# Optimization experiments

Hardware: AMD Instinct MI355X
Metric: run time of the kernel (lower is better)

Reference implementation:

```python
import jax, jax.numpy as jnp
import numpy as np

N_IN, N_LAT, LEN_T, N_SHIFT = 128, 21, 51, 50
N_HID, BATCH = 4, 2048


def identity_init(n_rows, n_cols):
    A = np.zeros((n_rows, n_cols), np.float32)
    if n_rows >= n_cols:
        k = n_rows - n_cols + 1
        for c in range(n_cols):
            A[c:c + k, c] = 1.0 / k
    else:
        k = n_cols - n_rows + 1
        for r in range(n_rows):
            A[r, r:r + k] = 1.0 / k
    return jnp.asarray(A)


def setup_inputs() -> dict:
    key = jax.random.key(0)
    ks = jax.random.split(key, 8)
    s = 0.05
    return {
        'inputs': jax.random.normal(ks[0], (BATCH, LEN_T, N_IN), dtype=jnp.float32),
        'enc_W': jax.random.normal(ks[1], (N_HID, N_IN, N_IN), dtype=jnp.float32) * s,
        'enc_b': jnp.zeros((N_HID, N_IN), jnp.float32),
        'enc_Wout': jax.random.normal(ks[2], (N_IN, N_IN), dtype=jnp.float32) * s,
        'enc_bout': jnp.zeros((N_IN,), jnp.float32),
        'dec_W': jax.random.normal(ks[3], (N_HID, N_IN, N_IN), dtype=jnp.float32) * s,
        'dec_b': jnp.zeros((N_HID, N_IN), jnp.float32),
        'dec_Wout': jax.random.normal(ks[4], (N_IN, N_IN), dtype=jnp.float32) * s,
        'dec_bout': jnp.zeros((N_IN,), jnp.float32),
        'W_enc_inner': identity_init(N_IN, N_LAT),
        'L': jnp.eye(N_LAT, dtype=jnp.float32),
        'W_dec_inner': identity_init(N_LAT, N_IN),
    }


def res_block(x, Ws, bs, Wout, bout):
    # DenseResBlock: ReLU hidden dense stack + linear output + identity skip
    h = x
    for i in range(Ws.shape[0]):
        h = jax.nn.relu(h @ Ws[i] + bs[i])
    return h @ Wout + bout + x


def reference(inputs, enc_W, enc_b, enc_Wout, enc_bout,
              dec_W, dec_b, dec_Wout, dec_bout,
              W_enc_inner, L, W_dec_inner):
    B = inputs.shape[0]
    len_pred = LEN_T - N_SHIFT  # = 1

    # ---- autoencoder branch (all timesteps flattened into rows) ----
    auto_in = inputs.reshape(-1, N_IN)                       # [B*T, n_in]
    part_enc = res_block(auto_in, enc_W, enc_b, enc_Wout, enc_bout)
    full_enc = part_enc @ W_enc_inner                        # [B*T, n_lat]
    part_dec = full_enc @ W_dec_inner                        # [B*T, n_in]
    autoencoder_output = res_block(part_dec, dec_W, dec_b, dec_Wout, dec_bout)
    autoencoder_output = autoencoder_output.reshape(B, LEN_T, N_IN)
    outer_auto_output = res_block(part_enc, dec_W, dec_b, dec_Wout, dec_bout)
    outer_auto_output = outer_auto_output.reshape(B, LEN_T, N_IN)

    # ---- prediction branch: recurrent application of Koopman operator L ----
    pred_in = inputs[:, :len_pred, :].reshape(-1, N_IN)      # [B*len_pred, n_in]
    cur = res_block(pred_in, enc_W, enc_b, enc_Wout, enc_bout) @ W_enc_inner

    def step(cur_enc, _):
        adv = cur_enc @ L                                    # [B*len_pred, n_lat]
        dec = res_block(adv @ W_dec_inner, dec_W, dec_b, dec_Wout, dec_bout)
        return adv, dec

    _, preds = jax.lax.scan(step, cur, None, length=N_SHIFT)  # [S, B*lp, n_in]
    preds = preds.reshape(N_SHIFT, B, len_pred, N_IN)
    predictions = preds.transpose(1, 0, 2, 3).reshape(B, N_SHIFT * len_pred, N_IN)

    return autoencoder_output, outer_auto_output, predictions
```

## Files before the change

kernel.cpp:

```cpp
#include <hip/hip_runtime.h>
#include <stdint.h>


typedef _Float16 h8 __attribute__((ext_vector_type(8)));
typedef _Float16 h4 __attribute__((ext_vector_type(4)));
typedef float    f4 __attribute__((ext_vector_type(4)));

#define ROWS_AUTO 104448
#define NT64      1632
#define NUNITS    1952

#define WT_ENCW      0
#define WT_ENCWOUT   (4*16384)
#define WT_DECW      (5*16384)
#define WT_DECWOUT   (9*16384)
#define WT_COMB      (10*16384)

#define MFULL_OFF_B 0x60000
#define ACH_OFF_B   0x200000
#define PE_OFF_B    0x220000
#define PET0_OFF_B  0x1C00000

#define H0 0
#define H1 16384
#define H2 32768
#define H3 49152
#define LDSE 51712
#define LDSD 68096

#define hsw(rl, c) ((rl)*256 + ((((c)) ^ ((rl) & 7)) << 4))

#define PIN(B) asm volatile("" : "+v"(B[0]), "+v"(B[1]), "+v"(B[2]), "+v"(B[3]), \
                                 "+v"(B[4]), "+v"(B[5]), "+v"(B[6]), "+v"(B[7]))

__device__ __forceinline__ f4 mfma16(h8 a, h8 b, f4 c) {
  return __builtin_amdgcn_mfma_f32_16x16x32_f16(a, b, c, 0, 0, 0);
}
__device__ __forceinline__ h8 cvt8(f4 a, f4 b) {
  h8 r;
  r[0]=(_Float16)a[0]; r[1]=(_Float16)a[1]; r[2]=(_Float16)a[2]; r[3]=(_Float16)a[3];
  r[4]=(_Float16)b[0]; r[5]=(_Float16)b[1]; r[6]=(_Float16)b[2]; r[7]=(_Float16)b[3];
  return r;
}
__device__ __forceinline__ void loadW(h8 B[8], const _Float16* gW, int nbase, int r15, int hi) {
#pragma unroll
  for (int nt = 0; nt < 2; ++nt)
#pragma unroll
    for (int ks = 0; ks < 4; ++ks)
      B[nt*4+ks] = *(const h8*)(gW + (size_t)(nbase + nt*16 + r15)*128 + ks*32 + hi*8);
}

__device__ __forceinline__ void mmF4s(const char* sm, int hb, const h8 B[8],
                                      f4 acc[4][2], int r15, int hi) {
#pragma unroll
  for (int rt = 0; rt < 4; ++rt) { acc[rt][0] = (f4){0,0,0,0}; acc[rt][1] = (f4){0,0,0,0}; }
#pragma unroll
  for (int ks = 0; ks < 4; ++ks) {
    int c = ks*4 + hi;
    h8 a[4];
#pragma unroll
    for (int rt = 0; rt < 4; ++rt) a[rt] = *(const h8*)(sm + hb + hsw(rt*16 + r15, c));
#pragma unroll
    for (int rt = 0; rt < 4; ++rt) {
      acc[rt][0] = mfma16(B[ks],   a[rt], acc[rt][0]);
      acc[rt][1] = mfma16(B[4+ks], a[rt], acc[rt][1]);
    }
  }
}

__device__ __forceinline__ void hw4s(char* sm, int hb, int wbase, const f4 acc[4][2],
                                     const float* bl, int bo, int r15, int hi) {
  f4 bb0 = *(const f4*)(bl + bo + wbase + hi*4);
  f4 bb1 = *(const f4*)(bl + bo + wbase + 16 + hi*4);
  int bo2 = (hi & 1) * 8;
#pragma unroll
  for (int nt = 0; nt < 2; ++nt) {
    int c = ((wbase + nt*16) >> 3) + (hi >> 1);
    f4 bb = nt ? bb1 : bb0;
#pragma unroll
    for (int rt = 0; rt < 4; ++rt) {
      int row = rt*16 + r15;
      h4 p;
#pragma unroll
      for (int d = 0; d < 4; ++d) p[d] = (_Float16)fmaxf(acc[rt][nt][d] + bb[d], 0.f);
      *(h4*)(sm + hb + row*256 + ((c ^ (row & 7)) << 4) + bo2) = p;
    }
  }
}
__device__ __forceinline__ void hw4r(char* sm, int hb, int wbase, const f4 acc[4][2],
                                     int r15, int hi) {
  int bo2 = (hi & 1) * 8;
#pragma unroll
  for (int nt = 0; nt < 2; ++nt) {
    int c = ((wbase + nt*16) >> 3) + (hi >> 1);
#pragma unroll
    for (int rt = 0; rt < 4; ++rt) {
      int row = rt*16 + r15;
      h4 p;
#pragma unroll
      for (int d = 0; d < 4; ++d) p[d] = (_Float16)acc[rt][nt][d];
      *(h4*)(sm + hb + row*256 + ((c ^ (row & 7)) << 4) + bo2) = p;
    }
  }
}

__device__ __forceinline__ void epi_store(char* sm, int hskip, int htr, int wbase,
                                          const f4 acc[4][2], const float* bl,
                                          float* dst, int rstride,
                                          int tid, int r15, int hi) {
  f4 bb0 = *(const f4*)(bl + 512 + wbase + hi*4);
  f4 bb1 = *(const f4*)(bl + 512 + wbase + 16 + hi*4);
  int bo2 = (hi & 1) * 8;
#pragma unroll
  for (int nt = 0; nt < 2; ++nt) {
    int c = ((wbase + nt*16) >> 3) + (hi >> 1);
    int q = (wbase >> 2) + nt*4 + hi;
    f4 bb = nt ? bb1 : bb0;
#pragma unroll
    for (int rt = 0; rt < 4; ++rt) {
      int row = rt*16 + r15;
      h4 sk = *(const h4*)(sm + hskip + row*256 + ((c ^ (row & 7)) << 4) + bo2);
      f4 v;
#pragma unroll
      for (int d = 0; d < 4; ++d) v[d] = acc[rt][nt][d] + bb[d] + (float)sk[d];
      *(f4*)(sm + htr + row*512 + ((q ^ ((row & 7) << 2)) << 4)) = v;
    }
  }
  __syncthreads();
#pragma unroll
  for (int i = 0; i < 8; ++i) {
    int idx = i*256 + tid, row = idx >> 5, q = idx & 31;
    f4 v = *(const f4*)(sm + htr + row*512 + ((q ^ ((row & 7) << 2)) << 4));
    *(f4*)(dst + (size_t)row*rstride + q*4) = v;
  }
}

#define LAYD(HIN, HOUT, BW, BO) do {                                 \
    mmF4s(sm, HIN, BW, acc, r15, hi);                                \
    hw4s(sm, HOUT, wbase, acc, bl, BO, r15, hi);                     \
    __syncthreads();                                                 \
  } while (0)


__global__ __launch_bounds__(512) void k_prep(
    const float* __restrict__ encW, const float* __restrict__ encWout,
    const float* __restrict__ decW, const float* __restrict__ decWout,
    const float* __restrict__ L,
    _Float16* __restrict__ wt, float* __restrict__ ach) {
  __shared__ float chA[441], chB[441];
  int m = blockIdx.y, tid = threadIdx.x;
  if (m == 10) {
    if (blockIdx.x != 0) return;
    if (tid < 441) chA[tid] = L[tid];
    __syncthreads();
    for (int s = 0; s < 50; ++s) {
      if (tid < 441) ach[s*441 + tid] = chA[tid];
      if (s == 49) break;
      if (tid < 441) {
        int i = tid / 21, j = tid % 21; float a = 0.f;
        for (int k = 0; k < 21; ++k) a += chA[i*21 + k] * L[k*21 + j];
        chB[tid] = a;
      }
      __syncthreads();
      if (tid < 441) chA[tid] = chB[tid];
      __syncthreads();
    }
    return;
  }
  int idx = blockIdx.x*512 + tid;
  if (idx >= 16384) return;
  const float* src; _Float16* dst;
  if (m < 4)       { src = encW + m*16384;     dst = wt + WT_ENCW + m*16384; }
  else if (m == 4) { src = encWout;            dst = wt + WT_ENCWOUT; }
  else if (m < 9)  { src = decW + (m-5)*16384; dst = wt + WT_DECW + (m-5)*16384; }
  else             { src = decWout;            dst = wt + WT_DECWOUT; }
  int n = idx >> 7, k = idx & 127;
  dst[idx] = (_Float16)src[k*128 + n];
}

__global__ __launch_bounds__(512) void k_aux(
    const float* __restrict__ ach, const float* __restrict__ wencI,
    const float* __restrict__ wdecI,
    _Float16* __restrict__ mfull, _Float16* __restrict__ wt) {
  __shared__ float T1[2688];
  __shared__ float sa[441];
  int s = blockIdx.x, t = threadIdx.x;
  if (s < 50) {
    if (t < 441) sa[t] = ach[s*441 + t];
    __syncthreads();
    for (int idx = t; idx < 2688; idx += 512) {
      int k = idx / 21, j = idx % 21;
      float a = 0.f;
      for (int u = 0; u < 21; ++u) a += wencI[k*21 + u] * sa[u*21 + j];
      T1[idx] = a;
    }
  } else {
    for (int idx = t; idx < 2688; idx += 512) T1[idx] = wencI[idx];
  }
  __syncthreads();
  _Float16* dst = (s < 50) ? (mfull + (size_t)s*16384) : (wt + WT_COMB);
  for (int idx = t; idx < 16384; idx += 512) {
    int n = idx >> 7, k = idx & 127;
    float a = 0.f;
    for (int j = 0; j < 21; ++j) a += T1[k*21 + j] * wdecI[j*128 + n];
    dst[idx] = (_Float16)a;
  }
}


__global__ __launch_bounds__(256, 2) void k_enc(
    const float* __restrict__ x, const _Float16* __restrict__ wt,
    const float* __restrict__ enc_b, const float* __restrict__ enc_bout,
    _Float16* __restrict__ pe_ws, _Float16* __restrict__ pet0) {
  __shared__ char sm[LDSE];
  float* bl = (float*)(sm + 49152);
  int tid = threadIdx.x, lane = tid & 63;
  int r15 = lane & 15, hi = lane >> 4;
  int wbase = (tid >> 6) * 32;
  h8 B0[8], B1[8], B2[8], B3[8], B4[8];
  loadW(B0, wt + WT_ENCW,           wbase, r15, hi);
  loadW(B1, wt + WT_ENCW + 16384,   wbase, r15, hi);
  loadW(B2, wt + WT_ENCW + 2*16384, wbase, r15, hi);
  loadW(B3, wt + WT_ENCW + 3*16384, wbase, r15, hi);
  loadW(B4, wt + WT_ENCWOUT,        wbase, r15, hi);
  PIN(B0); PIN(B1); PIN(B2); PIN(B3); PIN(B4);
  bl[tid] = enc_b[tid]; bl[256 + tid] = enc_b[256 + tid];
  if (tid < 128) bl[512 + tid] = enc_bout[tid];
  f4 acc[4][2];

  for (int t = blockIdx.x; t < NT64; t += gridDim.x) {
    size_t rb = (size_t)t * 64;
#pragma unroll
    for (int i = 0; i < 4; ++i) {
      int idx = i*256 + tid, rl = idx >> 4, c = idx & 15;
      const float* s = x + (rb + rl)*128 + c*8;
      f4 v0 = *(const f4*)s, v1 = *(const f4*)(s + 4);
      *(h8*)(sm + H0 + hsw(rl, c)) = cvt8(v0, v1);
    }
    __syncthreads();
    LAYD(H0, H1, B0, 0); LAYD(H1, H2, B1, 128);
    LAYD(H2, H1, B2, 256); LAYD(H1, H2, B3, 384);
    mmF4s(sm, H2, B4, acc, r15, hi);
    {
      f4 bb0 = *(const f4*)(bl + 512 + wbase + hi*4);
      f4 bb1 = *(const f4*)(bl + 512 + wbase + 16 + hi*4);
      int bo2 = (hi & 1) * 8;
#pragma unroll
      for (int nt = 0; nt < 2; ++nt) {
        int c = ((wbase + nt*16) >> 3) + (hi >> 1);
        f4 bb = nt ? bb1 : bb0;
#pragma unroll
        for (int rt = 0; rt < 4; ++rt) {
          int row = rt*16 + r15;
          int soff = row*256 + ((c ^ (row & 7)) << 4) + bo2;
          h4 sk = *(const h4*)(sm + H0 + soff);
          h4 p;
#pragma unroll
          for (int d = 0; d < 4; ++d) p[d] = (_Float16)(acc[rt][nt][d] + bb[d] + (float)sk[d]);
          *(h4*)(sm + H1 + soff) = p;
        }
      }
    }
    __syncthreads();
    {
      char* g = (char*)(pe_ws) + (size_t)t*16384;
#pragma unroll
      for (int i = 0; i < 4; ++i) {
        int idx = i*256 + tid, off = idx*16;
        f4 v = *(const f4*)(sm + H1 + off);
        *(f4*)(g + off) = v;
        int rl = idx >> 4, slot = idx & 15;
        size_t rg = rb + (size_t)rl;
        if (rg % 51u == 0u) {
          int c = slot ^ (rl & 7);
          *(f4*)((char*)pet0 + (rg/51u)*256 + c*16) = v;
        }
      }
    }
  }
}


__global__ __launch_bounds__(256, 2) void k_decpred(
    const _Float16* __restrict__ wt, const _Float16* __restrict__ pe_ws,
    const _Float16* __restrict__ pet0, const _Float16* __restrict__ mfull,
    const float* __restrict__ dec_b, const float* __restrict__ dec_bout,
    float* __restrict__ out1, float* __restrict__ out2, float* __restrict__ out3) {
  __shared__ char sm[LDSD];
  float* bl = (float*)(sm + 65536);
  int tid = threadIdx.x, lane = tid & 63;
  int r15 = lane & 15, hi = lane >> 4;
  int wbase = (tid >> 6) * 32;
  h8 B0[8], B1[8], B2[8], B3[8], B4[8];
  loadW(B0, wt + WT_DECW,           wbase, r15, hi);
  loadW(B1, wt + WT_DECW + 16384,   wbase, r15, hi);
  loadW(B2, wt + WT_DECW + 2*16384, wbase, r15, hi);
  loadW(B3, wt + WT_DECW + 3*16384, wbase, r15, hi);
  loadW(B4, wt + WT_DECWOUT,        wbase, r15, hi);
  PIN(B0); PIN(B1); PIN(B2); PIN(B3); PIN(B4);
  bl[tid] = dec_b[tid]; bl[256 + tid] = dec_b[256 + tid];
  if (tid < 128) bl[512 + tid] = dec_bout[tid];
  f4 acc[4][2];

  for (int u = blockIdx.x; u < NUNITS; u += gridDim.x) {
    __syncthreads();
    if (u < NT64) {
      const char* src = (const char*)pe_ws + (size_t)u*16384;
      float* d2 = out2 + (size_t)u*64*128;
      float* d1 = out1 + (size_t)u*64*128;
#pragma unroll
      for (int i = 0; i < 4; ++i) {
        int off = (i*256 + tid)*16;
        *(f4*)(sm + H0 + off) = *(const f4*)(src + off);
      }
      __syncthreads();
      LAYD(H0, H1, B0, 0); LAYD(H1, H2, B1, 128);
      LAYD(H2, H1, B2, 256); LAYD(H1, H2, B3, 384);
      mmF4s(sm, H2, B4, acc, r15, hi);
      __syncthreads();
      epi_store(sm, H0, H1, wbase, acc, bl, d2, 128, tid, r15, hi);
      {
        h8 Bc[8];
        loadW(Bc, wt + WT_COMB, wbase, r15, hi);
        mmF4s(sm, H0, Bc, acc, r15, hi);
      }
      hw4r(sm, H3, wbase, acc, r15, hi);
      __syncthreads();
      LAYD(H3, H0, B0, 0); LAYD(H0, H1, B1, 128);
      LAYD(H1, H0, B2, 256); LAYD(H0, H1, B3, 384);
      mmF4s(sm, H1, B4, acc, r15, hi);
      __syncthreads();
      epi_store(sm, H3, H0, wbase, acc, bl, d1, 128, tid, r15, hi);
    } else {
      int p = u - NT64, rtile = p / 10, chunk = p % 10;
#pragma unroll
      for (int i = 0; i < 4; ++i) {
        int idx = i*256 + tid, rl = idx >> 4, c = idx & 15;
        f4 v = *(const f4*)((const char*)pet0 + (size_t)(rtile*64 + rl)*256 + c*16);
        *(f4*)(sm + H0 + hsw(rl, c)) = v;
      }
      __syncthreads();
      for (int s = chunk*5; s < chunk*5 + 5; ++s) {
        {
          h8 Bm[8];
          loadW(Bm, mfull + (size_t)s*16384, wbase, r15, hi);
          mmF4s(sm, H0, Bm, acc, r15, hi);
        }
        hw4r(sm, H1, wbase, acc, r15, hi);
        __syncthreads();
        LAYD(H1, H2, B0, 0); LAYD(H2, H3, B1, 128);
        LAYD(H3, H2, B2, 256); LAYD(H2, H3, B3, 384);
        mmF4s(sm, H3, B4, acc, r15, hi);
        __syncthreads();
        epi_store(sm, H1, H2, wbase, acc, bl,
                  out3 + ((size_t)rtile*64*50 + s)*128, 50*128, tid, r15, hi);
        __syncthreads();
      }
    }
  }
}


extern "C" void kernel_launch(void* const* d_in, const int* in_sizes, int n_in,
                              void* d_out, int out_size, void* d_ws, size_t ws_size,
                              hipStream_t stream) {
  const float* x        = (const float*)d_in[0];
  const float* encW     = (const float*)d_in[1];
  const float* enc_b    = (const float*)d_in[2];
  const float* encWout  = (const float*)d_in[3];
  const float* enc_bout = (const float*)d_in[4];
  const float* decW     = (const float*)d_in[5];
  const float* dec_b    = (const float*)d_in[6];
  const float* decWout  = (const float*)d_in[7];
  const float* dec_bout = (const float*)d_in[8];
  const float* wencI    = (const float*)d_in[9];
  const float* L        = (const float*)d_in[10];
  const float* wdecI    = (const float*)d_in[11];

  char* ws = (char*)d_ws;
  _Float16* wt    = (_Float16*)ws;
  _Float16* mfull = (_Float16*)(ws + MFULL_OFF_B);
  float*    ach   = (float*)(ws + ACH_OFF_B);
  _Float16* pe_ws = (_Float16*)(ws + PE_OFF_B);
  _Float16* pet0  = (_Float16*)(ws + PET0_OFF_B);

  float* out1 = (float*)d_out;
  float* out2 = out1 + (size_t)ROWS_AUTO*128;
  float* out3 = out2 + (size_t)ROWS_AUTO*128;

  hipLaunchKernelGGL(k_prep, dim3(32, 11), dim3(512), 0, stream,
                     encW, encWout, decW, decWout, L, wt, ach);
  hipLaunchKernelGGL(k_aux, dim3(51), dim3(512), 0, stream,
                     ach, wencI, wdecI, mfull, wt);
  hipLaunchKernelGGL(k_enc, dim3(512), dim3(256), 0, stream,
                     x, wt, enc_b, enc_bout, pe_ws, pet0);
  hipLaunchKernelGGL(k_decpred, dim3(512), dim3(256), 0, stream,
                     wt, pe_ws, pet0, mfull, dec_b, dec_bout, out1, out2, out3);
}
```

Measured before the change: 224.6 us.

## Halve row tiles to 32 rows to raise occupancy in encoder and decoder kernels

Row tiles shrink from 64 to 32 rows, which halves the per-thread accumulators and the LDS buffers. Biases are now stored in LDS as fp16, and the combined weight is preloaded into registers in the decoder instead of being reloaded on every tile. Launch bounds and grid sizes rise to 6 and 4 blocks per CU, and the prediction work is split into 2-step chunks. The aim is better latency hiding through more resident waves. The cost is that each weight fragment is reused across fewer MFMAs, and there are more barriers per row processed. Holding biases in fp16 slightly reduces precision.

```diff
diff --git a/kernel.cpp b/kernel.cpp
--- a/kernel.cpp
+++ b/kernel.cpp
@@ -7,8 +7,8 @@
 typedef float    f4 __attribute__((ext_vector_type(4)));
 
 #define ROWS_AUTO 104448
-#define NT64      1632
-#define NUNITS    1952
+#define NT32      3264
+#define NUNITS    4864
 
 #define WT_ENCW      0
 #define WT_ENCWOUT   (4*16384)
@@ -21,12 +21,12 @@
 #define PE_OFF_B    0x220000
 #define PET0_OFF_B  0x1C00000
 
-#define H0 0
-#define H1 16384
-#define H2 32768
-#define H3 49152
-#define LDSE 51712
-#define LDSD 68096
+#define LA 0
+#define LB 8192
+#define LC 16384
+#define LD 24576
+#define LDSE (24576 + 1280)
+#define LDSD (32768 + 1280)
 
 #define hsw(rl, c) ((rl)*256 + ((((c)) ^ ((rl) & 7)) << 4))
 
@@ -50,51 +50,49 @@
       B[nt*4+ks] = *(const h8*)(gW + (size_t)(nbase + nt*16 + r15)*128 + ks*32 + hi*8);
 }
 
-__device__ __forceinline__ void mmF4s(const char* sm, int hb, const h8 B[8],
-                                      f4 acc[4][2], int r15, int hi) {
-#pragma unroll
-  for (int rt = 0; rt < 4; ++rt) { acc[rt][0] = (f4){0,0,0,0}; acc[rt][1] = (f4){0,0,0,0}; }
+__device__ __forceinline__ void mm(const char* sm, int hb, const h8 B[8],
+                                   f4 acc[2][2], int r15, int hi) {
+#pragma unroll
+  for (int rt = 0; rt < 2; ++rt) { acc[rt][0] = (f4){0,0,0,0}; acc[rt][1] = (f4){0,0,0,0}; }
 #pragma unroll
   for (int ks = 0; ks < 4; ++ks) {
     int c = ks*4 + hi;
-    h8 a[4];
-#pragma unroll
-    for (int rt = 0; rt < 4; ++rt) a[rt] = *(const h8*)(sm + hb + hsw(rt*16 + r15, c));
-#pragma unroll
-    for (int rt = 0; rt < 4; ++rt) {
-      acc[rt][0] = mfma16(B[ks],   a[rt], acc[rt][0]);
-      acc[rt][1] = mfma16(B[4+ks], a[rt], acc[rt][1]);
-    }
-  }
-}
-
-__device__ __forceinline__ void hw4s(char* sm, int hb, int wbase, const f4 acc[4][2],
-                                     const float* bl, int bo, int r15, int hi) {
-  f4 bb0 = *(const f4*)(bl + bo + wbase + hi*4);
-  f4 bb1 = *(const f4*)(bl + bo + wbase + 16 + hi*4);
+    h8 a0 = *(const h8*)(sm + hb + hsw(r15, c));
+    h8 a1 = *(const h8*)(sm + hb + hsw(16 + r15, c));
+    acc[0][0] = mfma16(B[ks],   a0, acc[0][0]);
+    acc[0][1] = mfma16(B[4+ks], a0, acc[0][1]);
+    acc[1][0] = mfma16(B[ks],   a1, acc[1][0]);
+    acc[1][1] = mfma16(B[4+ks], a1, acc[1][1]);
+  }
+}
+
+__device__ __forceinline__ void hws(char* sm, int hb, int wbase, const f4 acc[2][2],
+                                    const _Float16* blh, int bo, int r15, int hi) {
+  h4 b0 = *(const h4*)(blh + bo + wbase + hi*4);
+  h4 b1 = *(const h4*)(blh + bo + wbase + 16 + hi*4);
   int bo2 = (hi & 1) * 8;
 #pragma unroll
   for (int nt = 0; nt < 2; ++nt) {
     int c = ((wbase + nt*16) >> 3) + (hi >> 1);
-    f4 bb = nt ? bb1 : bb0;
-#pragma unroll
-    for (int rt = 0; rt < 4; ++rt) {
+    h4 bb = nt ? b1 : b0;
+#pragma unroll
+    for (int rt = 0; rt < 2; ++rt) {
       int row = rt*16 + r15;
       h4 p;
 #pragma unroll
-      for (int d = 0; d < 4; ++d) p[d] = (_Float16)fmaxf(acc[rt][nt][d] + bb[d], 0.f);
+      for (int d = 0; d < 4; ++d) p[d] = (_Float16)fmaxf(acc[rt][nt][d] + (float)bb[d], 0.f);
       *(h4*)(sm + hb + row*256 + ((c ^ (row & 7)) << 4) + bo2) = p;
     }
   }
 }
-__device__ __forceinline__ void hw4r(char* sm, int hb, int wbase, const f4 acc[4][2],
-                                     int r15, int hi) {
+__device__ __forceinline__ void hwa(char* sm, int hb, int wbase, const f4 acc[2][2],
+                                    int r15, int hi) {
   int bo2 = (hi & 1) * 8;
 #pragma unroll
   for (int nt = 0; nt < 2; ++nt) {
     int c = ((wbase + nt*16) >> 3) + (hi >> 1);
 #pragma unroll
-    for (int rt = 0; rt < 4; ++rt) {
+    for (int rt = 0; rt < 2; ++rt) {
       int row = rt*16 + r15;
       h4 p;
 #pragma unroll
@@ -104,41 +102,40 @@
   }
 }
 
-__device__ __forceinline__ void epi_store(char* sm, int hskip, int htr, int wbase,
-                                          const f4 acc[4][2], const float* bl,
-                                          float* dst, int rstride,
-                                          int tid, int r15, int hi) {
-  f4 bb0 = *(const f4*)(bl + 512 + wbase + hi*4);
-  f4 bb1 = *(const f4*)(bl + 512 + wbase + 16 + hi*4);
+__device__ __forceinline__ void epi(char* sm, int hskip, int trb, int wbase,
+                                    const f4 acc[2][2], const _Float16* blh, int bout,
+                                    float* dst, int rstride, int tid, int r15, int hi) {
+  h4 b0 = *(const h4*)(blh + bout + wbase + hi*4);
+  h4 b1 = *(const h4*)(blh + bout + wbase + 16 + hi*4);
   int bo2 = (hi & 1) * 8;
 #pragma unroll
   for (int nt = 0; nt < 2; ++nt) {
     int c = ((wbase + nt*16) >> 3) + (hi >> 1);
     int q = (wbase >> 2) + nt*4 + hi;
-    f4 bb = nt ? bb1 : bb0;
-#pragma unroll
-    for (int rt = 0; rt < 4; ++rt) {
+    h4 bb = nt ? b1 : b0;
+#pragma unroll
+    for (int rt = 0; rt < 2; ++rt) {
       int row = rt*16 + r15;
       h4 sk = *(const h4*)(sm + hskip + row*256 + ((c ^ (row & 7)) << 4) + bo2);
       f4 v;
 #pragma unroll
-      for (int d = 0; d < 4; ++d) v[d] = acc[rt][nt][d] + bb[d] + (float)sk[d];
-      *(f4*)(sm + htr + row*512 + ((q ^ ((row & 7) << 2)) << 4)) = v;
+      for (int d = 0; d < 4; ++d) v[d] = acc[rt][nt][d] + (float)bb[d] + (float)sk[d];
+      *(f4*)(sm + trb + row*512 + ((q ^ ((row & 7) << 2)) << 4)) = v;
     }
   }
   __syncthreads();
 #pragma unroll
-  for (int i = 0; i < 8; ++i) {
-    int idx = i*256 + tid, row = idx >> 5, q = idx & 31;
-    f4 v = *(const f4*)(sm + htr + row*512 + ((q ^ ((row & 7) << 2)) << 4));
-    *(f4*)(dst + (size_t)row*rstride + q*4) = v;
-  }
-}
-
-#define LAYD(HIN, HOUT, BW, BO) do {                                 \
-    mmF4s(sm, HIN, BW, acc, r15, hi);                                \
-    hw4s(sm, HOUT, wbase, acc, bl, BO, r15, hi);                     \
-    __syncthreads();                                                 \
+  for (int i = 0; i < 4; ++i) {
+    int idx = i*256 + tid, row = idx >> 5, qq = idx & 31;
+    f4 v = *(const f4*)(sm + trb + row*512 + ((qq ^ ((row & 7) << 2)) << 4));
+    *(f4*)(dst + (size_t)row*rstride + qq*4) = v;
+  }
+}
+
+#define LAYR(LIN, LOUT, BW, BO) do {                       \
+    mm(sm, LIN, BW, acc, r15, hi);                         \
+    hws(sm, LOUT, wbase, acc, blh, BO, r15, hi);           \
+    __syncthreads();                                       \
   } while (0)
 
 
@@ -208,12 +205,12 @@
 }
 
 
-__global__ __launch_bounds__(256, 2) void k_enc(
+__global__ __launch_bounds__(256, 6) void k_enc(
     const float* __restrict__ x, const _Float16* __restrict__ wt,
     const float* __restrict__ enc_b, const float* __restrict__ enc_bout,
     _Float16* __restrict__ pe_ws, _Float16* __restrict__ pet0) {
   __shared__ char sm[LDSE];
-  float* bl = (float*)(sm + 49152);
+  _Float16* blh = (_Float16*)(sm + 24576);
   int tid = threadIdx.x, lane = tid & 63;
   int r15 = lane & 15, hi = lane >> 4;
   int wbase = (tid >> 6) * 32;
@@ -224,50 +221,50 @@
   loadW(B3, wt + WT_ENCW + 3*16384, wbase, r15, hi);
   loadW(B4, wt + WT_ENCWOUT,        wbase, r15, hi);
   PIN(B0); PIN(B1); PIN(B2); PIN(B3); PIN(B4);
-  bl[tid] = enc_b[tid]; bl[256 + tid] = enc_b[256 + tid];
-  if (tid < 128) bl[512 + tid] = enc_bout[tid];
-  f4 acc[4][2];
-
-  for (int t = blockIdx.x; t < NT64; t += gridDim.x) {
-    size_t rb = (size_t)t * 64;
-#pragma unroll
-    for (int i = 0; i < 4; ++i) {
+  for (int i = tid; i < 640; i += 256)
+    blh[i] = (_Float16)(i < 512 ? enc_b[i] : enc_bout[i - 512]);
+  f4 acc[2][2];
+
+  for (int t = blockIdx.x; t < NT32; t += gridDim.x) {
+    size_t rb = (size_t)t * 32;
+#pragma unroll
+    for (int i = 0; i < 2; ++i) {
       int idx = i*256 + tid, rl = idx >> 4, c = idx & 15;
       const float* s = x + (rb + rl)*128 + c*8;
       f4 v0 = *(const f4*)s, v1 = *(const f4*)(s + 4);
-      *(h8*)(sm + H0 + hsw(rl, c)) = cvt8(v0, v1);
-    }
-    __syncthreads();
-    LAYD(H0, H1, B0, 0); LAYD(H1, H2, B1, 128);
-    LAYD(H2, H1, B2, 256); LAYD(H1, H2, B3, 384);
-    mmF4s(sm, H2, B4, acc, r15, hi);
+      *(h8*)(sm + LA + hsw(rl, c)) = cvt8(v0, v1);
+    }
+    __syncthreads();
+    LAYR(LA, LB, B0, 0); LAYR(LB, LC, B1, 128);
+    LAYR(LC, LB, B2, 256); LAYR(LB, LC, B3, 384);
+    mm(sm, LC, B4, acc, r15, hi);
     {
-      f4 bb0 = *(const f4*)(bl + 512 + wbase + hi*4);
-      f4 bb1 = *(const f4*)(bl + 512 + wbase + 16 + hi*4);
+      h4 bb0 = *(const h4*)(blh + 512 + wbase + hi*4);
+      h4 bb1 = *(const h4*)(blh + 512 + wbase + 16 + hi*4);
       int bo2 = (hi & 1) * 8;
 #pragma unroll
       for (int nt = 0; nt < 2; ++nt) {
         int c = ((wbase + nt*16) >> 3) + (hi >> 1);
-        f4 bb = nt ? bb1 : bb0;
-#pragma unroll
-        for (int rt = 0; rt < 4; ++rt) {
+        h4 bb = nt ? bb1 : bb0;
+#pragma unroll
+        for (int rt = 0; rt < 2; ++rt) {
           int row = rt*16 + r15;
-          int soff = row*256 + ((c ^ (row & 7)) << 4) + bo2;
-          h4 sk = *(const h4*)(sm + H0 + soff);
+          int soff = LA + row*256 + ((c ^ (row & 7)) << 4) + bo2;
+          h4 sk = *(const h4*)(sm + soff);
           h4 p;
 #pragma unroll
-          for (int d = 0; d < 4; ++d) p[d] = (_Float16)(acc[rt][nt][d] + bb[d] + (float)sk[d]);
-          *(h4*)(sm + H1 + soff) = p;
+          for (int d = 0; d < 4; ++d) p[d] = (_Float16)(acc[rt][nt][d] + (float)bb[d] + (float)sk[d]);
+          *(h4*)(sm + soff) = p;
         }
       }
     }
     __syncthreads();
     {
-      char* g = (char*)(pe_ws) + (size_t)t*16384;
-#pragma unroll
-      for (int i = 0; i < 4; ++i) {
+      char* g = (char*)(pe_ws) + (size_t)t*8192;
+#pragma unroll
+      for (int i = 0; i < 2; ++i) {
         int idx = i*256 + tid, off = idx*16;
-        f4 v = *(const f4*)(sm + H1 + off);
+        f4 v = *(const f4*)(sm + LA + off);
         *(f4*)(g + off) = v;
         int rl = idx >> 4, slot = idx & 15;
         size_t rg = rb + (size_t)rl;
@@ -277,83 +274,81 @@
         }
       }
     }
-  }
-}
-
-
-__global__ __launch_bounds__(256, 2) void k_decpred(
+    __syncthreads();
+  }
+}
+
+
+__global__ __launch_bounds__(256, 4) void k_decpred(
     const _Float16* __restrict__ wt, const _Float16* __restrict__ pe_ws,
     const _Float16* __restrict__ pet0, const _Float16* __restrict__ mfull,
     const float* __restrict__ dec_b, const float* __restrict__ dec_bout,
     float* __restrict__ out1, float* __restrict__ out2, float* __restrict__ out3) {
   __shared__ char sm[LDSD];
-  float* bl = (float*)(sm + 65536);
+  _Float16* blh = (_Float16*)(sm + 32768);
   int tid = threadIdx.x, lane = tid & 63;
   int r15 = lane & 15, hi = lane >> 4;
   int wbase = (tid >> 6) * 32;
-  h8 B0[8], B1[8], B2[8], B3[8], B4[8];
+  h8 B0[8], B1[8], B2[8], B3[8], B4[8], B5[8];
   loadW(B0, wt + WT_DECW,           wbase, r15, hi);
   loadW(B1, wt + WT_DECW + 16384,   wbase, r15, hi);
   loadW(B2, wt + WT_DECW + 2*16384, wbase, r15, hi);
   loadW(B3, wt + WT_DECW + 3*16384, wbase, r15, hi);
   loadW(B4, wt + WT_DECWOUT,        wbase, r15, hi);
-  PIN(B0); PIN(B1); PIN(B2); PIN(B3); PIN(B4);
-  bl[tid] = dec_b[tid]; bl[256 + tid] = dec_b[256 + tid];
-  if (tid < 128) bl[512 + tid] = dec_bout[tid];
-  f4 acc[4][2];
+  loadW(B5, wt + WT_COMB,           wbase, r15, hi);
+  PIN(B0); PIN(B1); PIN(B2); PIN(B3); PIN(B4); PIN(B5);
+  for (int i = tid; i < 640; i += 256)
+    blh[i] = (_Float16)(i < 512 ? dec_b[i] : dec_bout[i - 512]);
+  f4 acc[2][2];
 
   for (int u = blockIdx.x; u < NUNITS; u += gridDim.x) {
     __syncthreads();
-    if (u < NT64) {
-      const char* src = (const char*)pe_ws + (size_t)u*16384;
-      float* d2 = out2 + (size_t)u*64*128;
-      float* d1 = out1 + (size_t)u*64*128;
-#pragma unroll
-      for (int i = 0; i < 4; ++i) {
+    if (u < NT32) {
+      const char* src = (const char*)pe_ws + (size_t)u*8192;
+#pragma unroll
+      for (int i = 0; i < 2; ++i) {
         int off = (i*256 + tid)*16;
-        *(f4*)(sm + H0 + off) = *(const f4*)(src + off);
-      }
-      __syncthreads();
-      LAYD(H0, H1, B0, 0); LAYD(H1, H2, B1, 128);
-      LAYD(H2, H1, B2, 256); LAYD(H1, H2, B3, 384);
-      mmF4s(sm, H2, B4, acc, r15, hi);
-      __syncthreads();
-      epi_store(sm, H0, H1, wbase, acc, bl, d2, 128, tid, r15, hi);
-      {
-        h8 Bc[8];
-        loadW(Bc, wt + WT_COMB, wbase, r15, hi);
-        mmF4s(sm, H0, Bc, acc, r15, hi);
-      }
-      hw4r(sm, H3, wbase, acc, r15, hi);
-      __syncthreads();
-      LAYD(H3, H0, B0, 0); LAYD(H0, H1, B1, 128);
-      LAYD(H1, H0, B2, 256); LAYD(H0, H1, B3, 384);
-      mmF4s(sm, H1, B4, acc, r15, hi);
-      __syncthreads();
-      epi_store(sm, H3, H0, wbase, acc, bl, d1, 128, tid, r15, hi);
+        *(f4*)(sm + LA + off) = *(const f4*)(src + off);
+      }
+      __syncthreads();
+      LAYR(LA, LB, B0, 0); LAYR(LB, LC, B1, 128);
+      LAYR(LC, LB, B2, 256); LAYR(LB, LC, B3, 384);
+      mm(sm, LC, B4, acc, r15, hi);
+      __syncthreads();
+      epi(sm, LA, LB, wbase, acc, blh, 512,
+          out2 + (size_t)u*32*128, 128, tid, r15, hi);
+      mm(sm, LA, B5, acc, r15, hi);
+      hwa(sm, LD, wbase, acc, r15, hi);
+      __syncthreads();
+      LAYR(LD, LA, B0, 0); LAYR(LA, LB, B1, 128);
+      LAYR(LB, LC, B2, 256); LAYR(LC, LA, B3, 384);
+      mm(sm, LA, B4, acc, r15, hi);
+      __syncthreads();
+      epi(sm, LD, LB, wbase, acc, blh, 512,
+          out1 + (size_t)u*32*128, 128, tid, r15, hi);
     } else {
-      int p = u - NT64, rtile = p / 10, chunk = p % 10;
-#pragma unroll
-      for (int i = 0; i < 4; ++i) {
+      int p = u - NT32, rtile = p / 25, chunk = p % 25;
+#pragma unroll
+      for (int i = 0; i < 2; ++i) {
         int idx = i*256 + tid, rl = idx >> 4, c = idx & 15;
-        f4 v = *(const f4*)((const char*)pet0 + (size_t)(rtile*64 + rl)*256 + c*16);
-        *(f4*)(sm + H0 + hsw(rl, c)) = v;
-      }
-      __syncthreads();
-      for (int s = chunk*5; s < chunk*5 + 5; ++s) {
+        f4 v = *(const f4*)((const char*)pet0 + (size_t)(rtile*32 + rl)*256 + c*16);
+        *(f4*)(sm + LA + hsw(rl, c)) = v;
+      }
+      __syncthreads();
+      for (int s = chunk*2; s < chunk*2 + 2; ++s) {
         {
           h8 Bm[8];
           loadW(Bm, mfull + (size_t)s*16384, wbase, r15, hi);
-          mmF4s(sm, H0, Bm, acc, r15, hi);
+          mm(sm, LA, Bm, acc, r15, hi);
         }
-        hw4r(sm, H1, wbase, acc, r15, hi);
+        hwa(sm, LB, wbase, acc, r15, hi);
         __syncthreads();
-        LAYD(H1, H2, B0, 0); LAYD(H2, H3, B1, 128);
-        LAYD(H3, H2, B2, 256); LAYD(H2, H3, B3, 384);
-        mmF4s(sm, H3, B4, acc, r15, hi);
+        LAYR(LB, LC, B0, 0); LAYR(LC, LD, B1, 128);
+        LAYR(LD, LC, B2, 256); LAYR(LC, LD, B3, 384);
+        mm(sm, LD, B4, acc, r15, hi);
         __syncthreads();
-        epi_store(sm, H1, H2, wbase, acc, bl,
-                  out3 + ((size_t)rtile*64*50 + s)*128, 50*128, tid, r15, hi);
+        epi(sm, LB, LC, wbase, acc, blh, 512,
+            out3 + ((size_t)rtile*32*50 + s)*128, 50*128, tid, r15, hi);
         __syncthreads();
       }
     }
@@ -392,8 +387,8 @@
                      encW, encWout, decW, decWout, L, wt, ach);
   hipLaunchKernelGGL(k_aux, dim3(51), dim3(512), 0, stream,
                      ach, wencI, wdecI, mfull, wt);
-  hipLaunchKernelGGL(k_enc, dim3(512), dim3(256), 0, stream,
+  hipLaunchKernelGGL(k_enc, dim3(1536), dim3(256), 0, stream,
                      x, wt, enc_b, enc_bout, pe_ws, pet0);
-  hipLaunchKernelGGL(k_decpred, dim3(512), dim3(256), 0, stream,
+  hipLaunchKernelGGL(k_decpred, dim3(1024), dim3(256), 0, stream,
                      wt, pe_ws, pet0, mfull, dec_b, dec_bout, out1, out2, out3);
 }
```

Result: slower. 695.7 us (+209.7%).

## Store epilogue directly to global and split prediction work into finer units

Applied to the files above, without the earlier changes.

Replaces the LDS-transposed coalesced epilogue with direct per-lane f4 global stores, removing a barrier and an LDS round trip per output tile. Prediction units now cover 2 shift steps instead of 5, raising the unit count for better load balance. The encoder writes its result in place into H0, which shrinks LDS use, and adds a trailing barrier. Direct stores are less coalesced (16-byte segments scattered across rows), which could raise write traffic cost.

```diff
diff --git a/kernel.cpp b/kernel.cpp
--- a/kernel.cpp
+++ b/kernel.cpp
@@ -8,7 +8,7 @@
 
 #define ROWS_AUTO 104448
 #define NT64      1632
-#define NUNITS    1952
+#define NUNITS    2432
 
 #define WT_ENCW      0
 #define WT_ENCWOUT   (4*16384)
@@ -25,8 +25,8 @@
 #define H1 16384
 #define H2 32768
 #define H3 49152
-#define LDSE 51712
-#define LDSD 68096
+#define LDSE (49152 + 2560)
+#define LDSD (65536 + 2560)
 
 #define hsw(rl, c) ((rl)*256 + ((((c)) ^ ((rl) & 7)) << 4))
 
@@ -104,17 +104,16 @@
   }
 }
 
-__device__ __forceinline__ void epi_store(char* sm, int hskip, int htr, int wbase,
-                                          const f4 acc[4][2], const float* bl,
-                                          float* dst, int rstride,
-                                          int tid, int r15, int hi) {
+__device__ __forceinline__ void epi_direct(const char* sm, int hskip, int wbase,
+                                           const f4 acc[4][2], const float* bl,
+                                           float* dst, int rstride, int r15, int hi) {
   f4 bb0 = *(const f4*)(bl + 512 + wbase + hi*4);
   f4 bb1 = *(const f4*)(bl + 512 + wbase + 16 + hi*4);
   int bo2 = (hi & 1) * 8;
 #pragma unroll
   for (int nt = 0; nt < 2; ++nt) {
     int c = ((wbase + nt*16) >> 3) + (hi >> 1);
-    int q = (wbase >> 2) + nt*4 + hi;
+    int n0 = wbase + nt*16 + hi*4;
     f4 bb = nt ? bb1 : bb0;
 #pragma unroll
     for (int rt = 0; rt < 4; ++rt) {
@@ -123,15 +122,8 @@
       f4 v;
 #pragma unroll
       for (int d = 0; d < 4; ++d) v[d] = acc[rt][nt][d] + bb[d] + (float)sk[d];
-      *(f4*)(sm + htr + row*512 + ((q ^ ((row & 7) << 2)) << 4)) = v;
-    }
-  }
-  __syncthreads();
-#pragma unroll
-  for (int i = 0; i < 8; ++i) {
-    int idx = i*256 + tid, row = idx >> 5, q = idx & 31;
-    f4 v = *(const f4*)(sm + htr + row*512 + ((q ^ ((row & 7) << 2)) << 4));
-    *(f4*)(dst + (size_t)row*rstride + q*4) = v;
+      *(f4*)(dst + (size_t)row*rstride + n0) = v;
+    }
   }
 }
 
@@ -252,12 +244,12 @@
 #pragma unroll
         for (int rt = 0; rt < 4; ++rt) {
           int row = rt*16 + r15;
-          int soff = row*256 + ((c ^ (row & 7)) << 4) + bo2;
-          h4 sk = *(const h4*)(sm + H0 + soff);
+          int soff = H0 + row*256 + ((c ^ (row & 7)) << 4) + bo2;
+          h4 sk = *(const h4*)(sm + soff);
           h4 p;
 #pragma unroll
           for (int d = 0; d < 4; ++d) p[d] = (_Float16)(acc[rt][nt][d] + bb[d] + (float)sk[d]);
-          *(h4*)(sm + H1 + soff) = p;
+          *(h4*)(sm + soff) = p;
         }
       }
     }
@@ -267,7 +259,7 @@
 #pragma unroll
       for (int i = 0; i < 4; ++i) {
         int idx = i*256 + tid, off = idx*16;
-        f4 v = *(const f4*)(sm + H1 + off);
+        f4 v = *(const f4*)(sm + H0 + off);
         *(f4*)(g + off) = v;
         int rl = idx >> 4, slot = idx & 15;
         size_t rg = rb + (size_t)rl;
@@ -277,6 +269,7 @@
         }
       }
     }
+    __syncthreads();
   }
 }
 
@@ -306,8 +299,6 @@
     __syncthreads();
     if (u < NT64) {
       const char* src = (const char*)pe_ws + (size_t)u*16384;
-      float* d2 = out2 + (size_t)u*64*128;
-      float* d1 = out1 + (size_t)u*64*128;
 #pragma unroll
       for (int i = 0; i < 4; ++i) {
         int off = (i*256 + tid)*16;
@@ -317,8 +308,8 @@
       LAYD(H0, H1, B0, 0); LAYD(H1, H2, B1, 128);
       LAYD(H2, H1, B2, 256); LAYD(H1, H2, B3, 384);
       mmF4s(sm, H2, B4, acc, r15, hi);
-      __syncthreads();
-      epi_store(sm, H0, H1, wbase, acc, bl, d2, 128, tid, r15, hi);
+      epi_direct(sm, H0, wbase, acc, bl,
+                 out2 + (size_t)u*64*128, 128, r15, hi);
       {
         h8 Bc[8];
         loadW(Bc, wt + WT_COMB, wbase, r15, hi);
@@ -329,10 +320,10 @@
       LAYD(H3, H0, B0, 0); LAYD(H0, H1, B1, 128);
       LAYD(H1, H0, B2, 256); LAYD(H0, H1, B3, 384);
       mmF4s(sm, H1, B4, acc, r15, hi);
-      __syncthreads();
-      epi_store(sm, H3, H0, wbase, acc, bl, d1, 128, tid, r15, hi);
+      epi_direct(sm, H3, wbase, acc, bl,
+                 out1 + (size_t)u*64*128, 128, r15, hi);
     } else {
-      int p = u - NT64, rtile = p / 10, chunk = p % 10;
+      int p = u - NT64, rtile = p / 25, chunk = p % 25;
 #pragma unroll
       for (int i = 0; i < 4; ++i) {
         int idx = i*256 + tid, rl = idx >> 4, c = idx & 15;
@@ -340,7 +331,7 @@
         *(f4*)(sm + H0 + hsw(rl, c)) = v;
       }
       __syncthreads();
-      for (int s = chunk*5; s < chunk*5 + 5; ++s) {
+      for (int s = chunk*2; s < chunk*2 + 2; ++s) {
         {
           h8 Bm[8];
           loadW(Bm, mfull + (size_t)s*16384, wbase, r15, hi);
@@ -351,9 +342,8 @@
         LAYD(H1, H2, B0, 0); LAYD(H2, H3, B1, 128);
         LAYD(H3, H2, B2, 256); LAYD(H2, H3, B3, 384);
         mmF4s(sm, H3, B4, acc, r15, hi);
-        __syncthreads();
-        epi_store(sm, H1, H2, wbase, acc, bl,
-                  out3 + ((size_t)rtile*64*50 + s)*128, 50*128, tid, r15, hi);
+        epi_direct(sm, H1, wbase, acc, bl,
+                   out3 + ((size_t)rtile*64*50 + s)*128, 50*128, r15, hi);
         __syncthreads();
       }
     }
```

Result: faster. 198.2 us, median of 2 (-11.8%).
